# Optimization experiments

Hardware: AMD Instinct MI355X
Metric: run time of the kernel (lower is better)

Reference implementation:

```python
import jax, jax.numpy as jnp
import numpy as np

T, B, S, L = 256, 128, 256, 2
H, E, V = 512, 512, 32000


def setup_inputs() -> dict:
    key = jax.random.key(0)
    ks = jax.random.split(key, 17)
    n = lambda k, shape, s=0.05: jax.random.normal(k, shape, dtype=jnp.float32) * s
    tokens = jax.random.randint(ks[0], (T, B), 0, V)
    emb = n(ks[1], (V, E)).at[0].set(0.0)  # padding_idx=0 row zeroed
    return {
        "tokens": tokens,
        "h0": n(ks[2], (L, B, H)),
        "c0": n(ks[3], (L, B, H)),
        "context": n(ks[4], (S, B, H)),
        "init_output": n(ks[5], (B, H)),
        "emb": emb,
        "W_ih0": n(ks[6], (4 * H, E + H)),
        "b_ih0": n(ks[7], (4 * H,)),
        "W_hh0": n(ks[8], (4 * H, H)),
        "b_hh0": n(ks[9], (4 * H,)),
        "W_ih1": n(ks[10], (4 * H, H)),
        "b_ih1": n(ks[11], (4 * H,)),
        "W_hh1": n(ks[12], (4 * H, H)),
        "b_hh1": n(ks[13], (4 * H,)),
        "W_in": n(ks[14], (H, H)),
        "W_out": n(ks[15], (H, 2 * H)),
    }


def _lstm_cell(x, h, c, Wi, bi, Wh, bh):
    # torch LSTMCell: gates ordered i, f, g, o
    g = x @ Wi.T + bi + h @ Wh.T + bh
    i, f, gg, o = jnp.split(g, 4, axis=-1)
    c2 = jax.nn.sigmoid(f) * c + jax.nn.sigmoid(i) * jnp.tanh(gg)
    h2 = jax.nn.sigmoid(o) * jnp.tanh(c2)
    return h2, c2


def reference(tokens, h0, c0, context, init_output, emb,
              W_ih0, b_ih0, W_hh0, b_hh0, W_ih1, b_ih1, W_hh1, b_hh1,
              W_in, W_out):
    emb_seq = emb[tokens]                      # [T, B, E]
    ctx = jnp.transpose(context, (1, 0, 2))    # [B, S, H] (context.transpose(0,1))

    def step(carry, e_t):
        h, c, out = carry                      # h,c: [L,B,H]; out: [B,H]
        x = jnp.concatenate([e_t, out], axis=1)  # input feed
        h0_, c0_ = _lstm_cell(x, h[0], c[0], W_ih0, b_ih0, W_hh0, b_hh0)
        h1_, c1_ = _lstm_cell(h0_, h[1], c[1], W_ih1, b_ih1, W_hh1, b_hh1)
        rnn_out = h1_                          # dropout is identity at p=0 / eval
        # GlobalAttention (Luong general): score = ctx @ (W_in h)
        q = rnn_out @ W_in.T                   # [B, H]
        scores = jnp.einsum('bsh,bh->bs', ctx, q)
        a = jax.nn.softmax(scores, axis=-1)    # [B, S]
        wc = jnp.einsum('bs,bsh->bh', a, ctx)  # weighted context
        attn_out = jnp.tanh(jnp.concatenate([wc, rnn_out], axis=1) @ W_out.T)
        new_h = jnp.stack([h0_, h1_])
        new_c = jnp.stack([c0_, c1_])
        return (new_h, new_c, attn_out), (attn_out, a)

    (hF, cF, _), (outputs, attns) = jax.lax.scan(step, (h0, c0, init_output), emb_seq)
    return outputs, hF, cF, attns[-1]
```

## Files before the change

### kernel.cpp

```cpp
#include <hip/hip_runtime.h>
#include <hip/hip_bf16.h>
#include <math.h>

#define TT 256
#define BB 128
#define SS 256
#define HH 512
#define EE 512
#define NBLK 128
#define NTHR 512
#define BH (BB * HH)

typedef __attribute__((ext_vector_type(4))) float f32x4;
typedef __attribute__((ext_vector_type(2))) float f32x2;
typedef __attribute__((ext_vector_type(8))) short s16x8;
typedef unsigned long long u64;

__device__ __forceinline__ float b2f(short v) {
    union { unsigned u; float f; } c;
    c.u = ((unsigned)(unsigned short)v) << 16;
    return c.f;
}
__device__ __forceinline__ short f2b(float f) {
    union { float f; unsigned u; } c; c.f = f;
    unsigned u = c.u;
    unsigned r = (u + 0x7fffu + ((u >> 16) & 1u)) >> 16;
    return (short)r;
}
__device__ __forceinline__ float sigm(float x) { return 1.f / (1.f + __expf(-x)); }

__device__ __forceinline__ unsigned short f2fp8x2(float x, float y) {
    return (unsigned short)(__builtin_amdgcn_cvt_pk_fp8_f32(x, y, 0, false) & 0xffff);
}
__device__ __forceinline__ void f8x8(u64 q, float* o) {
    unsigned w0 = (unsigned)q, w1 = (unsigned)(q >> 32);
    f32x2 a = __builtin_amdgcn_cvt_pk_f32_fp8(w0, false);
    f32x2 b = __builtin_amdgcn_cvt_pk_f32_fp8(w0, true);
    f32x2 c = __builtin_amdgcn_cvt_pk_f32_fp8(w1, false);
    f32x2 d = __builtin_amdgcn_cvt_pk_f32_fp8(w1, true);
    o[0] = a[0]; o[1] = a[1]; o[2] = b[0]; o[3] = b[1];
    o[4] = c[0]; o[5] = c[1]; o[6] = d[0]; o[7] = d[1];
}

__device__ __forceinline__ u64 aldq(const void* p) {
    return __hip_atomic_load((const u64*)p, __ATOMIC_RELAXED, __HIP_MEMORY_SCOPE_AGENT);
}
__device__ __forceinline__ void ast2(short* p, short v) {
    __hip_atomic_store(p, v, __ATOMIC_RELAXED, __HIP_MEMORY_SCOPE_AGENT);
}
__device__ __forceinline__ s16x8 ald16(const void* p) {
    s16x8 r;
    asm volatile("global_load_dwordx4 %0, %1, off sc0 sc1" : "=v"(r) : "v"(p) : "memory");
    return r;
}


__global__ void k_pack2(const float* __restrict__ Wa, int ka, const float* __restrict__ Wb, int kb,
                        short* __restrict__ dst, int n) {
    const int K = ka + kb;
    for (int i = blockIdx.x * blockDim.x + threadIdx.x; i < n; i += gridDim.x * blockDim.x) {
        int g = i / K, k = i - g * K;
        float v = (k < ka) ? Wa[(size_t)g * ka + k] : Wb[(size_t)g * kb + (k - ka)];
        dst[i] = f2b(v);
    }
}

__global__ void k_bias(const float* __restrict__ a, const float* __restrict__ b, float* __restrict__ o,
                       const float* __restrict__ a2, const float* __restrict__ b2, float* __restrict__ o2) {
    int i = blockIdx.x * blockDim.x + threadIdx.x;
    if (i < 2048) { o[i] = a[i] + b[i]; o2[i] = a2[i] + b2[i]; }
}

__global__ void k_emb(const int* __restrict__ tok, const float* __restrict__ emb, short* __restrict__ Ebf) {
    const int n = TT * BB * EE;
    for (int i = blockIdx.x * blockDim.x + threadIdx.x; i < n; i += gridDim.x * blockDim.x) {
        int tb = i >> 9, k = i & 511;
        int t = tok[tb];
        Ebf[i] = f2b(emb[(size_t)t * EE + k]);
    }
}

__global__ void k_ctx8(const float* __restrict__ ctx, unsigned char* __restrict__ c8) {
    const int n2 = BB * SS * (HH / 2);
    for (int i = blockIdx.x * blockDim.x + threadIdx.x; i < n2; i += gridDim.x * blockDim.x) {
        int h2 = i & 255, rest = i >> 8;
        int s = rest & 255, b = rest >> 8;
        int h = h2 * 2;
        const float* src = ctx + ((size_t)s * BB + b) * HH + h;
        *reinterpret_cast<unsigned short*>(c8 + ((size_t)b * SS + s) * HH + h) = f2fp8x2(src[0], src[1]);
    }
}

__global__ __launch_bounds__(512) void k_ctxw8(const float* __restrict__ ctx, const short* __restrict__ Winb,
                                               unsigned char* __restrict__ ctxW8) {
    const int tid = threadIdx.x, w = tid >> 6, l = tid & 63;
    const int m0 = blockIdx.y * 128, n0 = blockIdx.x * 64;
    const int kc8 = (l >> 4) * 8;
    const int m = m0 + w * 16 + (l & 15);
    const int b = m >> 8, s = m & 255;
    const float* arow = ctx + ((size_t)s * BB + b) * HH + kc8;
    f32x4 acc[4];
    const f32x4 zero = {0.f, 0.f, 0.f, 0.f};
#pragma unroll
    for (int j = 0; j < 4; ++j) acc[j] = zero;
#pragma unroll
    for (int kc = 0; kc < 16; ++kc) {
        const int k0 = kc * 32;
        float4 x0 = *reinterpret_cast<const float4*>(arow + k0);
        float4 x1 = *reinterpret_cast<const float4*>(arow + k0 + 4);
        s16x8 afr;
        afr[0] = f2b(x0.x); afr[1] = f2b(x0.y); afr[2] = f2b(x0.z); afr[3] = f2b(x0.w);
        afr[4] = f2b(x1.x); afr[5] = f2b(x1.y); afr[6] = f2b(x1.z); afr[7] = f2b(x1.w);
#pragma unroll
        for (int j = 0; j < 4; ++j) {
            s16x8 bfr = *reinterpret_cast<const s16x8*>(Winb + (size_t)(n0 + j * 16 + (l & 15)) * HH + k0 + kc8);
            acc[j] = __builtin_amdgcn_mfma_f32_16x16x32_bf16(afr, bfr, acc[j], 0, 0, 0);
        }
    }
#pragma unroll
    for (int j = 0; j < 4; ++j)
#pragma unroll
        for (int r = 0; r < 4; ++r)
            ctxW8[(size_t)(m0 + w * 16 + (l >> 4) * 4 + r) * HH + (n0 + j * 16 + (l & 15))] =
                (unsigned char)(__builtin_amdgcn_cvt_pk_fp8_f32(acc[j][r], 0.f, 0, false) & 0xff);
}

__global__ void k_state(const float* __restrict__ h0in, const float* __restrict__ iout,
                        short* __restrict__ h0x, short* __restrict__ h1x, short* __restrict__ outx) {
    int i = blockIdx.x * blockDim.x + threadIdx.x;
    if (i < BH) {
        h0x[i] = f2b(h0in[i]);
        h1x[i] = f2b(h0in[BH + i]);
        outx[i] = f2b(iout[i]);
    }
}


struct P {
    const short* Ebf;
    const float* c0in;
    const unsigned char* ctxb8;
    const unsigned char* ctxW8;
    const short* W0cat;
    const short* W1cat;
    const short* Woutb;
    const float* bias0;
    const float* bias1;
    short* h0x;
    short* h1x;
    short* outx;
    short* wcx;
    float* dout;
    unsigned* flags;
};

#define MFMA16(a, b, c) __builtin_amdgcn_mfma_f32_16x16x32_bf16((a), (b), (c), 0, 0, 0)

__device__ __forceinline__ s16x8 ldsfrag(const short* base, int stride, int row, int col8) {
    return *reinterpret_cast<const s16x8*>(base + row * stride + ((col8 ^ (row & 7)) << 3));
}

__device__ __forceinline__ void issue8(const short* __restrict__ src, int tid, int khalf, s16x8* q) {
#pragma unroll
    for (int c = 0; c < 8; ++c) {
        const int chunk = c * 512 + tid;
        const int row = chunk >> 5, col8 = chunk & 31;
        q[c] = ald16(src + row * HH + khalf * 256 + col8 * 8);
    }
}
__device__ __forceinline__ void write8(short* __restrict__ stg, int tid, const s16x8* q) {
    asm volatile("s_waitcnt vmcnt(0)" ::: "memory");
#pragma unroll
    for (int c = 0; c < 8; ++c) {
        const int chunk = c * 512 + tid;
        const int row = chunk >> 5, col8 = chunk & 31;
        *reinterpret_cast<s16x8*>(stg + row * 256 + ((col8 ^ (row & 7)) << 3)) = q[c];
    }
}

__device__ __forceinline__ f32x4 seg8(const short* stgp, const short* Ws, int wstride, int wbase,
                                      int mrow, int wrow, int kq, f32x4 acc) {
#pragma unroll
    for (int seg = 0; seg < 8; ++seg)
        acc = MFMA16(ldsfrag(stgp, 256, mrow, seg * 4 + kq),
                     ldsfrag(Ws, wstride, wrow, wbase + seg * 4 + kq), acc);
    return acc;
}

__device__ __forceinline__ f32x4 seg8m(const short* stgp, const short* Wd, int wbase,
                                       int mrow, int nn, int kq, bool valid, f32x4 acc) {
    const s16x8 zz = {0, 0, 0, 0, 0, 0, 0, 0};
#pragma unroll
    for (int seg = 0; seg < 8; ++seg) {
        s16x8 b = ldsfrag(Wd, 1024, nn & 3, wbase + seg * 4 + kq);
        if (!valid) b = zz;
        acc = MFMA16(ldsfrag(stgp, 256, mrow, seg * 4 + kq), b, acc);
    }
    return acc;
}

__device__ __forceinline__ void gbar(unsigned* flags, unsigned target) {
    asm volatile("s_waitcnt vmcnt(0)" ::: "memory");
    __syncthreads();
    if (threadIdx.x == 0)
        __hip_atomic_store(&flags[blockIdx.x], target, __ATOMIC_RELAXED, __HIP_MEMORY_SCOPE_AGENT);
    if (threadIdx.x < NBLK) {
        while (__hip_atomic_load(&flags[threadIdx.x], __ATOMIC_RELAXED, __HIP_MEMORY_SCOPE_AGENT) < target)
            __builtin_amdgcn_s_sleep(1);
    }
    __syncthreads();
}

__global__ void __launch_bounds__(NTHR, 1) coop_k(P p) {
    extern __shared__ __align__(16) char smem[];
    short* W0s = (short*)smem;
    short* W1s = W0s + 16 * 1536;
    short* Wds = W1s + 16 * 1024;
    short* stg = Wds + 4 * 1024;
    float* smallf = (float*)(stg + 128 * 256);
    float* bias0s = smallf;
    float* bias1s = smallf + 16;
    float* red = smallf + 32;
    float* scv = smallf + 48;
    float* aU = smallf + 304;

    const int tid = threadIdx.x;
    const int blk = blockIdx.x;
    const int l = tid & 63;
    const int w = tid >> 6;
    const int lrow = l & 15;
    const int mrow = w * 16 + lrow;
    const int kq = l >> 4;
    const size_t OFF_HF = (size_t)TT * BH;
    const size_t OFF_CF = OFF_HF + 2 * (size_t)BH;
    const size_t OFF_AT = OFF_CF + 2 * (size_t)BH;
    const f32x4 fz = {0.f, 0.f, 0.f, 0.f};

    for (int idx = tid; idx < 16 * 192; idx += NTHR) {
        int row = idx / 192, col8 = idx % 192;
        int g = (row & 3) * 512 + blk * 4 + (row >> 2);
        *reinterpret_cast<s16x8*>(W0s + row * 1536 + ((col8 ^ (row & 7)) << 3)) =
            *reinterpret_cast<const s16x8*>(p.W0cat + (size_t)g * 1536 + col8 * 8);
    }
    for (int idx = tid; idx < 16 * 128; idx += NTHR) {
        int row = idx / 128, col8 = idx % 128;
        int g = (row & 3) * 512 + blk * 4 + (row >> 2);
        *reinterpret_cast<s16x8*>(W1s + row * 1024 + ((col8 ^ (row & 7)) << 3)) =
            *reinterpret_cast<const s16x8*>(p.W1cat + (size_t)g * 1024 + col8 * 8);
    }
    {
        int row = tid >> 7, col8 = tid & 127;
        *reinterpret_cast<s16x8*>(Wds + row * 1024 + ((col8 ^ row) << 3)) =
            *reinterpret_cast<const s16x8*>(p.Woutb + (size_t)(blk * 4 + row) * 1024 + col8 * 8);
    }
    if (tid < 16) {
        int g = (tid & 3) * 512 + blk * 4 + (tid >> 2);
        bias0s[tid] = p.bias0[g];
        bias1s[tid] = p.bias1[g];
    }
    __syncthreads();

    const int bA = tid >> 2;
    const int jA = blk * 4 + (tid & 3);
    float c0reg = p.c0in[bA * HH + jA];
    float c1reg = p.c0in[BH + bA * HH + jA];
    unsigned ep = 0;
    s16x8 qa[8], qb[8];

    for (int t = 0; t < TT; ++t) {
        const size_t pB = (size_t)(t & 1) * BH;
        const size_t pN = (size_t)((t & 1) ^ 1) * BH;

        {
            issue8(p.outx + pB, tid, 0, qa);
            f32x4 aE = fz, aO = fz, aH = fz;
            {
                const short* erow = p.Ebf + ((size_t)t * BB + mrow) * EE + kq * 8;
#pragma unroll
                for (int seg = 0; seg < 16; ++seg) {
                    s16x8 afr = *reinterpret_cast<const s16x8*>(erow + seg * 32);
                    aE = MFMA16(afr, ldsfrag(W0s, 1536, lrow, seg * 4 + kq), aE);
                }
            }
            write8(stg, tid, qa);
            issue8(p.outx + pB, tid, 1, qb);
            __syncthreads();
            aO = seg8(stg, W0s, 1536, 64, mrow, lrow, kq, aO);
            __syncthreads();
            write8(stg, tid, qb);
            issue8(p.h0x + pB, tid, 0, qa);
            __syncthreads();
            aO = seg8(stg, W0s, 1536, 96, mrow, lrow, kq, aO);
            __syncthreads();
            write8(stg, tid, qa);
            issue8(p.h0x + pB, tid, 1, qb);
            __syncthreads();
            aH = seg8(stg, W0s, 1536, 128, mrow, lrow, kq, aH);
            __syncthreads();
            write8(stg, tid, qb);
            __syncthreads();
            aH = seg8(stg, W0s, 1536, 160, mrow, lrow, kq, aH);

            f32x4 acc = aE + aO + aH;
            __syncthreads();
            float* scr = (float*)stg + w * 272;
#pragma unroll
            for (int r = 0; r < 4; ++r) scr[lrow * 17 + kq * 4 + r] = acc[r];
            __syncthreads();
            const int bloc = l >> 2;
            const int n0 = (l & 3) * 4;
            float gi = scr[(n0 + 0) * 17 + bloc] + bias0s[n0 + 0];
            float gf = scr[(n0 + 1) * 17 + bloc] + bias0s[n0 + 1];
            float gg = scr[(n0 + 2) * 17 + bloc] + bias0s[n0 + 2];
            float go = scr[(n0 + 3) * 17 + bloc] + bias0s[n0 + 3];
            float cn = sigm(gf) * c0reg + sigm(gi) * tanhf(gg);
            float hn = sigm(go) * tanhf(cn);
            c0reg = cn;
            ast2(&p.h0x[pN + bA * HH + jA], f2b(hn));
            if (t == TT - 1) {
                p.dout[OFF_HF + bA * HH + jA] = hn;
                p.dout[OFF_CF + bA * HH + jA] = cn;
            }
        }
        gbar(p.flags, ++ep);

        {
            issue8(p.h0x + pN, tid, 0, qa);
            f32x4 b0 = fz, b1 = fz;
            write8(stg, tid, qa);
            issue8(p.h0x + pN, tid, 1, qb);
            __syncthreads();
            b0 = seg8(stg, W1s, 1024, 0, mrow, lrow, kq, b0);
            __syncthreads();
            write8(stg, tid, qb);
            issue8(p.h1x + pB, tid, 0, qa);
            __syncthreads();
            b0 = seg8(stg, W1s, 1024, 32, mrow, lrow, kq, b0);
            __syncthreads();
            write8(stg, tid, qa);
            issue8(p.h1x + pB, tid, 1, qb);
            __syncthreads();
            b1 = seg8(stg, W1s, 1024, 64, mrow, lrow, kq, b1);
            __syncthreads();
            write8(stg, tid, qb);
            __syncthreads();
            b1 = seg8(stg, W1s, 1024, 96, mrow, lrow, kq, b1);

            f32x4 acc = b0 + b1;
            __syncthreads();
            float* scr = (float*)stg + w * 272;
#pragma unroll
            for (int r = 0; r < 4; ++r) scr[lrow * 17 + kq * 4 + r] = acc[r];
            __syncthreads();
            const int bloc = l >> 2;
            const int n0 = (l & 3) * 4;
            float gi = scr[(n0 + 0) * 17 + bloc] + bias1s[n0 + 0];
            float gf = scr[(n0 + 1) * 17 + bloc] + bias1s[n0 + 1];
            float gg = scr[(n0 + 2) * 17 + bloc] + bias1s[n0 + 2];
            float go = scr[(n0 + 3) * 17 + bloc] + bias1s[n0 + 3];
            float cn = sigm(gf) * c1reg + sigm(gi) * tanhf(gg);
            float hn = sigm(go) * tanhf(cn);
            c1reg = cn;
            ast2(&p.h1x[pN + bA * HH + jA], f2b(hn));
            if (t == TT - 1) {
                p.dout[OFF_HF + BH + bA * HH + jA] = hn;
                p.dout[OFF_CF + BH + bA * HH + jA] = cn;
            }
        }
        gbar(p.flags, ++ep);

        {
            float* pF = (float*)stg;
            float* h1f = pF + 4096;
            if (tid < 128) {
                union { u64 v; short s[4]; } c;
                c.v = aldq(p.h1x + pN + blk * HH + tid * 4);
#pragma unroll
                for (int j = 0; j < 4; ++j) h1f[tid * 4 + j] = b2f(c.s[j]);
            }
            __syncthreads();
            float hreg[8];
#pragma unroll
            for (int j = 0; j < 8; ++j) hreg[j] = h1f[l * 8 + j];
            const unsigned char* cwb = p.ctxW8 + (size_t)blk * SS * HH;
#pragma unroll 4
            for (int it = 0; it < 32; ++it) {
                const int s = it * 8 + w;
                u64 q = *reinterpret_cast<const u64*>(cwb + (size_t)s * HH + l * 8);
                float o[8];
                f8x8(q, o);
                float pd = 0.f;
#pragma unroll
                for (int j = 0; j < 8; ++j) pd += o[j] * hreg[j];
#pragma unroll
                for (int off = 32; off; off >>= 1) pd += __shfl_xor(pd, off);
                if (l == 0) scv[s] = pd;
            }
            __syncthreads();
            float sc = -1e30f, e = 0.f;
            if (tid < 256) sc = scv[tid];
            float mx = sc;
#pragma unroll
            for (int off = 32; off; off >>= 1) mx = fmaxf(mx, __shfl_xor(mx, off));
            if (l == 0 && tid < 256) red[w] = mx;
            __syncthreads();
            const float M = fmaxf(fmaxf(red[0], red[1]), fmaxf(red[2], red[3]));
            if (tid < 256) { e = __expf(sc - M); aU[tid] = e; }
            float se = e;
#pragma unroll
            for (int off = 32; off; off >>= 1) se += __shfl_xor(se, off);
            if (l == 0 && tid < 256) red[8 + w] = se;
            __syncthreads();
            const float inv = 1.f / (red[8] + red[9] + red[10] + red[11]);
            if (t == TT - 1 && tid < 256) p.dout[OFF_AT + blk * SS + tid] = aU[tid] * inv;
            const unsigned char* cbb = p.ctxb8 + (size_t)blk * SS * HH;
            float wa[8];
#pragma unroll
            for (int j = 0; j < 8; ++j) wa[j] = 0.f;
#pragma unroll 4
            for (int it = 0; it < 32; ++it) {
                const int s = it * 8 + w;
                const float av = aU[s];
                u64 q = *reinterpret_cast<const u64*>(cbb + (size_t)s * HH + l * 8);
                float o[8];
                f8x8(q, o);
#pragma unroll
                for (int j = 0; j < 8; ++j) wa[j] += av * o[j];
            }
            {
                float4* dst = reinterpret_cast<float4*>(pF + w * 512 + l * 8);
                float4 v0 = {wa[0], wa[1], wa[2], wa[3]};
                float4 v1 = {wa[4], wa[5], wa[6], wa[7]};
                dst[0] = v0;
                dst[1] = v1;
            }
            __syncthreads();
            float s8 = 0.f;
#pragma unroll
            for (int ww = 0; ww < 8; ++ww) s8 += pF[ww * 512 + tid];
            ast2(&p.wcx[blk * HH + tid], f2b(s8 * inv));
        }
        gbar(p.flags, ++ep);

        {
            issue8(p.wcx, tid, 0, qa);
            f32x4 acc = fz;
            const int nn = l & 15;
            const bool dv = nn < 4;
            write8(stg, tid, qa);
            issue8(p.wcx, tid, 1, qb);
            __syncthreads();
            acc = seg8m(stg, Wds, 0, mrow, nn, kq, dv, acc);
            __syncthreads();
            write8(stg, tid, qb);
            issue8(p.h1x + pN, tid, 0, qa);
            __syncthreads();
            acc = seg8m(stg, Wds, 32, mrow, nn, kq, dv, acc);
            __syncthreads();
            write8(stg, tid, qa);
            issue8(p.h1x + pN, tid, 1, qb);
            __syncthreads();
            acc = seg8m(stg, Wds, 64, mrow, nn, kq, dv, acc);
            __syncthreads();
            write8(stg, tid, qb);
            __syncthreads();
            acc = seg8m(stg, Wds, 96, mrow, nn, kq, dv, acc);
            if (dv) {
                const int col = blk * 4 + nn;
#pragma unroll
                for (int r = 0; r < 4; ++r) {
                    const int row = w * 16 + (l >> 4) * 4 + r;
                    float tv = tanhf(acc[r]);
                    __builtin_nontemporal_store(tv, &p.dout[(size_t)t * BH + row * HH + col]);
                    ast2(&p.outx[pN + row * HH + col], f2b(tv));
                }
            }
        }
        gbar(p.flags, ++ep);
    }
}


extern "C" void kernel_launch(void* const* d_in, const int* in_sizes, int n_in,
                              void* d_out, int out_size, void* d_ws, size_t ws_size,
                              hipStream_t stream) {
    const int* tokens = (const int*)d_in[0];
    const float* h0in = (const float*)d_in[1];
    const float* c0in = (const float*)d_in[2];
    const float* ctx = (const float*)d_in[3];
    const float* iout = (const float*)d_in[4];
    const float* emb = (const float*)d_in[5];
    const float* Wih0 = (const float*)d_in[6];
    const float* bih0 = (const float*)d_in[7];
    const float* Whh0 = (const float*)d_in[8];
    const float* bhh0 = (const float*)d_in[9];
    const float* Wih1 = (const float*)d_in[10];
    const float* bih1 = (const float*)d_in[11];
    const float* Whh1 = (const float*)d_in[12];
    const float* bhh1 = (const float*)d_in[13];
    const float* Win = (const float*)d_in[14];
    const float* Wout = (const float*)d_in[15];
    float* dout = (float*)d_out;

    char* pw = (char*)d_ws;
    auto take = [&](size_t bytes) { char* r = pw; pw += (bytes + 255) & ~(size_t)255; return r; };
    short* W0cat = (short*)take((size_t)2048 * 1536 * 2);
    short* W1cat = (short*)take((size_t)2048 * 1024 * 2);
    short* Winb  = (short*)take((size_t)512 * 512 * 2);
    short* Woutb = (short*)take((size_t)512 * 1024 * 2);
    float* bias0 = (float*)take(2048 * 4);
    float* bias1 = (float*)take(2048 * 4);
    short* Ebf   = (short*)take((size_t)TT * BB * EE * 2);
    unsigned char* ctxb8 = (unsigned char*)take((size_t)BB * SS * HH);
    unsigned char* ctxW8 = (unsigned char*)take((size_t)BB * SS * HH);
    short* h0x   = (short*)take((size_t)2 * BH * 2);
    short* h1x   = (short*)take((size_t)2 * BH * 2);
    short* outx  = (short*)take((size_t)2 * BH * 2);
    short* wcx   = (short*)take((size_t)BH * 2);
    unsigned* flags = (unsigned*)take(NBLK * 4);

    k_pack2<<<2048, 256, 0, stream>>>(Wih0, 1024, Whh0, 512, W0cat, 2048 * 1536);
    k_pack2<<<2048, 256, 0, stream>>>(Wih1, 512, Whh1, 512, W1cat, 2048 * 1024);
    k_pack2<<<1024, 256, 0, stream>>>(Win, 512, Win, 0, Winb, 512 * 512);
    k_pack2<<<1024, 256, 0, stream>>>(Wout, 1024, Wout, 0, Woutb, 512 * 1024);
    k_bias<<<8, 256, 0, stream>>>(bih0, bhh0, bias0, bih1, bhh1, bias1);
    k_emb<<<4096, 256, 0, stream>>>(tokens, emb, Ebf);
    k_ctx8<<<4096, 256, 0, stream>>>(ctx, ctxb8);
    k_state<<<256, 256, 0, stream>>>(h0in, iout, h0x, h1x, outx);
    k_ctxw8<<<dim3(8, 256), 512, 0, stream>>>(ctx, Winb, ctxW8);
    (void)hipMemsetAsync(flags, 0, NBLK * 4, stream);

    const unsigned smem_bytes = (16 * 1536 + 16 * 1024 + 4 * 1024 + 128 * 256) * 2 + (16 + 16 + 16 + 256 + 256) * 4;
    (void)hipFuncSetAttribute((const void*)coop_k, hipFuncAttributeMaxDynamicSharedMemorySize, (int)smem_bytes);

    P prm;
    prm.Ebf = Ebf; prm.c0in = c0in;
    prm.ctxb8 = ctxb8; prm.ctxW8 = ctxW8;
    prm.W0cat = W0cat; prm.W1cat = W1cat; prm.Woutb = Woutb;
    prm.bias0 = bias0; prm.bias1 = bias1;
    prm.h0x = h0x; prm.h1x = h1x; prm.outx = outx; prm.wcx = wcx;
    prm.dout = dout; prm.flags = flags;
    void* args[] = {&prm};
    (void)hipLaunchCooperativeKernel((void*)coop_k, dim3(NBLK), dim3(NTHR), args, smem_bytes, stream);
}
```

Measured before the change: 15.08 ms.

## Precompute ctx·W_out context projection to drop one grid barrier per step

The context half of the output projection is folded into a precomputed fp8 tensor, ctx @ W_out[:, :H].T, built by the generalized k_cvt8 kernel. Each block now forms its batch row's attention output directly as the attention-weighted sum of this projected context plus an h1·W_out_r dot product read from a packed bf16 buffer. This removes the separate output-projection phase and its grid-wide barrier each timestep. It also replaces many __syncthreads with lighter LDS-only barriers and prefetches more global loads ahead of time, at the cost of more precomputed memory and extra fp8 quantization error.

```diff
diff --git a/kernel.cpp b/kernel.cpp
--- a/kernel.cpp
+++ b/kernel.cpp
@@ -54,6 +54,11 @@
     return r;
 }
 
+__device__ __forceinline__ void lbar() {
+    asm volatile("s_waitcnt lgkmcnt(0)" ::: "memory");
+    __builtin_amdgcn_s_barrier();
+}
+
 
 __global__ void k_pack2(const float* __restrict__ Wa, int ka, const float* __restrict__ Wb, int kb,
                         short* __restrict__ dst, int n) {
@@ -80,19 +85,18 @@
     }
 }
 
-__global__ void k_ctx8(const float* __restrict__ ctx, unsigned char* __restrict__ c8) {
-    const int n2 = BB * SS * (HH / 2);
-    for (int i = blockIdx.x * blockDim.x + threadIdx.x; i < n2; i += gridDim.x * blockDim.x) {
-        int h2 = i & 255, rest = i >> 8;
-        int s = rest & 255, b = rest >> 8;
-        int h = h2 * 2;
-        const float* src = ctx + ((size_t)s * BB + b) * HH + h;
-        *reinterpret_cast<unsigned short*>(c8 + ((size_t)b * SS + s) * HH + h) = f2fp8x2(src[0], src[1]);
-    }
-}
-
-__global__ __launch_bounds__(512) void k_ctxw8(const float* __restrict__ ctx, const short* __restrict__ Winb,
-                                               unsigned char* __restrict__ ctxW8) {
+__global__ void k_packwr(const float* __restrict__ Wout, unsigned* __restrict__ WRP) {
+    int i = blockIdx.x * blockDim.x + threadIdx.x;
+    if (i < 256 * 512) {
+        int m = i >> 9, j = i & 511;
+        unsigned lo = (unsigned)(unsigned short)f2b(Wout[(size_t)j * 1024 + 512 + 2 * m]);
+        unsigned hi = (unsigned)(unsigned short)f2b(Wout[(size_t)j * 1024 + 512 + 2 * m + 1]);
+        WRP[i] = lo | (hi << 16);
+    }
+}
+
+__global__ __launch_bounds__(512) void k_cvt8(const float* __restrict__ ctx, const short* __restrict__ Wb,
+                                              int wstride, unsigned char* __restrict__ out8) {
     const int tid = threadIdx.x, w = tid >> 6, l = tid & 63;
     const int m0 = blockIdx.y * 128, n0 = blockIdx.x * 64;
     const int kc8 = (l >> 4) * 8;
@@ -113,7 +117,7 @@
         afr[4] = f2b(x1.x); afr[5] = f2b(x1.y); afr[6] = f2b(x1.z); afr[7] = f2b(x1.w);
 #pragma unroll
         for (int j = 0; j < 4; ++j) {
-            s16x8 bfr = *reinterpret_cast<const s16x8*>(Winb + (size_t)(n0 + j * 16 + (l & 15)) * HH + k0 + kc8);
+            s16x8 bfr = *reinterpret_cast<const s16x8*>(Wb + (size_t)(n0 + j * 16 + (l & 15)) * wstride + k0 + kc8);
             acc[j] = __builtin_amdgcn_mfma_f32_16x16x32_bf16(afr, bfr, acc[j], 0, 0, 0);
         }
     }
@@ -121,7 +125,7 @@
     for (int j = 0; j < 4; ++j)
 #pragma unroll
         for (int r = 0; r < 4; ++r)
-            ctxW8[(size_t)(m0 + w * 16 + (l >> 4) * 4 + r) * HH + (n0 + j * 16 + (l & 15))] =
+            out8[(size_t)(m0 + w * 16 + (l >> 4) * 4 + r) * HH + (n0 + j * 16 + (l & 15))] =
                 (unsigned char)(__builtin_amdgcn_cvt_pk_fp8_f32(acc[j][r], 0.f, 0, false) & 0xff);
 }
 
@@ -139,17 +143,16 @@
 struct P {
     const short* Ebf;
     const float* c0in;
-    const unsigned char* ctxb8;
     const unsigned char* ctxW8;
+    const unsigned char* ctxO8;
+    const unsigned* WRP;
     const short* W0cat;
     const short* W1cat;
-    const short* Woutb;
     const float* bias0;
     const float* bias1;
     short* h0x;
     short* h1x;
     short* outx;
-    short* wcx;
     float* dout;
     unsigned* flags;
 };
@@ -168,8 +171,9 @@
         q[c] = ald16(src + row * HH + khalf * 256 + col8 * 8);
     }
 }
-__device__ __forceinline__ void write8(short* __restrict__ stg, int tid, const s16x8* q) {
-    asm volatile("s_waitcnt vmcnt(0)" ::: "memory");
+template <int N>
+__device__ __forceinline__ void write8n(short* __restrict__ stg, int tid, const s16x8* q) {
+    asm volatile("s_waitcnt vmcnt(%0)" ::"i"(N) : "memory");
 #pragma unroll
     for (int c = 0; c < 8; ++c) {
         const int chunk = c * 512 + tid;
@@ -184,18 +188,6 @@
     for (int seg = 0; seg < 8; ++seg)
         acc = MFMA16(ldsfrag(stgp, 256, mrow, seg * 4 + kq),
                      ldsfrag(Ws, wstride, wrow, wbase + seg * 4 + kq), acc);
-    return acc;
-}
-
-__device__ __forceinline__ f32x4 seg8m(const short* stgp, const short* Wd, int wbase,
-                                       int mrow, int nn, int kq, bool valid, f32x4 acc) {
-    const s16x8 zz = {0, 0, 0, 0, 0, 0, 0, 0};
-#pragma unroll
-    for (int seg = 0; seg < 8; ++seg) {
-        s16x8 b = ldsfrag(Wd, 1024, nn & 3, wbase + seg * 4 + kq);
-        if (!valid) b = zz;
-        acc = MFMA16(ldsfrag(stgp, 256, mrow, seg * 4 + kq), b, acc);
-    }
     return acc;
 }
 
@@ -215,14 +207,14 @@
     extern __shared__ __align__(16) char smem[];
     short* W0s = (short*)smem;
     short* W1s = W0s + 16 * 1536;
-    short* Wds = W1s + 16 * 1024;
-    short* stg = Wds + 4 * 1024;
+    short* stg = W1s + 16 * 1024;
     float* smallf = (float*)(stg + 128 * 256);
     float* bias0s = smallf;
     float* bias1s = smallf + 16;
     float* red = smallf + 32;
     float* scv = smallf + 48;
     float* aU = smallf + 304;
+    float* h1f = smallf + 560;
 
     const int tid = threadIdx.x;
     const int blk = blockIdx.x;
@@ -248,11 +240,6 @@
         *reinterpret_cast<s16x8*>(W1s + row * 1024 + ((col8 ^ (row & 7)) << 3)) =
             *reinterpret_cast<const s16x8*>(p.W1cat + (size_t)g * 1024 + col8 * 8);
     }
-    {
-        int row = tid >> 7, col8 = tid & 127;
-        *reinterpret_cast<s16x8*>(Wds + row * 1024 + ((col8 ^ row) << 3)) =
-            *reinterpret_cast<const s16x8*>(p.Woutb + (size_t)(blk * 4 + row) * 1024 + col8 * 8);
-    }
     if (tid < 16) {
         int g = (tid & 3) * 512 + blk * 4 + (tid >> 2);
         bias0s[tid] = p.bias0[g];
@@ -265,7 +252,7 @@
     float c0reg = p.c0in[bA * HH + jA];
     float c1reg = p.c0in[BH + bA * HH + jA];
     unsigned ep = 0;
-    s16x8 qa[8], qb[8];
+    s16x8 qa[8], qb[8], qc[8], qd[8];
 
     for (int t = 0; t < TT; ++t) {
         const size_t pB = (size_t)(t & 1) * BH;
@@ -273,6 +260,7 @@
 
         {
             issue8(p.outx + pB, tid, 0, qa);
+            issue8(p.outx + pB, tid, 1, qb);
             f32x4 aE = fz, aO = fz, aH = fz;
             {
                 const short* erow = p.Ebf + ((size_t)t * BB + mrow) * EE + kq * 8;
@@ -282,31 +270,29 @@
                     aE = MFMA16(afr, ldsfrag(W0s, 1536, lrow, seg * 4 + kq), aE);
                 }
             }
-            write8(stg, tid, qa);
-            issue8(p.outx + pB, tid, 1, qb);
-            __syncthreads();
+            write8n<8>(stg, tid, qa);
+            issue8(p.h0x + pB, tid, 0, qc);
+            lbar();
             aO = seg8(stg, W0s, 1536, 64, mrow, lrow, kq, aO);
-            __syncthreads();
-            write8(stg, tid, qb);
-            issue8(p.h0x + pB, tid, 0, qa);
-            __syncthreads();
+            lbar();
+            write8n<8>(stg, tid, qb);
+            issue8(p.h0x + pB, tid, 1, qd);
+            lbar();
             aO = seg8(stg, W0s, 1536, 96, mrow, lrow, kq, aO);
-            __syncthreads();
-            write8(stg, tid, qa);
-            issue8(p.h0x + pB, tid, 1, qb);
-            __syncthreads();
+            lbar();
+            write8n<8>(stg, tid, qc);
+            lbar();
             aH = seg8(stg, W0s, 1536, 128, mrow, lrow, kq, aH);
-            __syncthreads();
-            write8(stg, tid, qb);
-            __syncthreads();
+            lbar();
+            write8n<0>(stg, tid, qd);
+            lbar();
             aH = seg8(stg, W0s, 1536, 160, mrow, lrow, kq, aH);
 
             f32x4 acc = aE + aO + aH;
-            __syncthreads();
+            lbar();
             float* scr = (float*)stg + w * 272;
 #pragma unroll
             for (int r = 0; r < 4; ++r) scr[lrow * 17 + kq * 4 + r] = acc[r];
-            __syncthreads();
             const int bloc = l >> 2;
             const int n0 = (l & 3) * 4;
             float gi = scr[(n0 + 0) * 17 + bloc] + bias0s[n0 + 0];
@@ -326,32 +312,31 @@
 
         {
             issue8(p.h0x + pN, tid, 0, qa);
+            issue8(p.h0x + pN, tid, 1, qb);
             f32x4 b0 = fz, b1 = fz;
-            write8(stg, tid, qa);
-            issue8(p.h0x + pN, tid, 1, qb);
-            __syncthreads();
+            write8n<8>(stg, tid, qa);
+            issue8(p.h1x + pB, tid, 0, qc);
+            lbar();
             b0 = seg8(stg, W1s, 1024, 0, mrow, lrow, kq, b0);
-            __syncthreads();
-            write8(stg, tid, qb);
-            issue8(p.h1x + pB, tid, 0, qa);
-            __syncthreads();
+            lbar();
+            write8n<8>(stg, tid, qb);
+            issue8(p.h1x + pB, tid, 1, qd);
+            lbar();
             b0 = seg8(stg, W1s, 1024, 32, mrow, lrow, kq, b0);
-            __syncthreads();
-            write8(stg, tid, qa);
-            issue8(p.h1x + pB, tid, 1, qb);
-            __syncthreads();
+            lbar();
+            write8n<8>(stg, tid, qc);
+            lbar();
             b1 = seg8(stg, W1s, 1024, 64, mrow, lrow, kq, b1);
-            __syncthreads();
-            write8(stg, tid, qb);
-            __syncthreads();
+            lbar();
+            write8n<0>(stg, tid, qd);
+            lbar();
             b1 = seg8(stg, W1s, 1024, 96, mrow, lrow, kq, b1);
 
             f32x4 acc = b0 + b1;
-            __syncthreads();
+            lbar();
             float* scr = (float*)stg + w * 272;
 #pragma unroll
             for (int r = 0; r < 4; ++r) scr[lrow * 17 + kq * 4 + r] = acc[r];
-            __syncthreads();
             const int bloc = l >> 2;
             const int n0 = (l & 3) * 4;
             float gi = scr[(n0 + 0) * 17 + bloc] + bias1s[n0 + 0];
@@ -371,14 +356,13 @@
 
         {
             float* pF = (float*)stg;
-            float* h1f = pF + 4096;
             if (tid < 128) {
                 union { u64 v; short s[4]; } c;
                 c.v = aldq(p.h1x + pN + blk * HH + tid * 4);
 #pragma unroll
                 for (int j = 0; j < 4; ++j) h1f[tid * 4 + j] = b2f(c.s[j]);
             }
-            __syncthreads();
+            lbar();
             float hreg[8];
 #pragma unroll
             for (int j = 0; j < 8; ++j) hreg[j] = h1f[l * 8 + j];
@@ -396,24 +380,24 @@
                 for (int off = 32; off; off >>= 1) pd += __shfl_xor(pd, off);
                 if (l == 0) scv[s] = pd;
             }
-            __syncthreads();
+            lbar();
             float sc = -1e30f, e = 0.f;
             if (tid < 256) sc = scv[tid];
             float mx = sc;
 #pragma unroll
             for (int off = 32; off; off >>= 1) mx = fmaxf(mx, __shfl_xor(mx, off));
             if (l == 0 && tid < 256) red[w] = mx;
-            __syncthreads();
+            lbar();
             const float M = fmaxf(fmaxf(red[0], red[1]), fmaxf(red[2], red[3]));
             if (tid < 256) { e = __expf(sc - M); aU[tid] = e; }
             float se = e;
 #pragma unroll
             for (int off = 32; off; off >>= 1) se += __shfl_xor(se, off);
             if (l == 0 && tid < 256) red[8 + w] = se;
-            __syncthreads();
+            lbar();
             const float inv = 1.f / (red[8] + red[9] + red[10] + red[11]);
             if (t == TT - 1 && tid < 256) p.dout[OFF_AT + blk * SS + tid] = aU[tid] * inv;
-            const unsigned char* cbb = p.ctxb8 + (size_t)blk * SS * HH;
+            const unsigned char* cob = p.ctxO8 + (size_t)blk * SS * HH;
             float wa[8];
 #pragma unroll
             for (int j = 0; j < 8; ++j) wa[j] = 0.f;
@@ -421,7 +405,7 @@
             for (int it = 0; it < 32; ++it) {
                 const int s = it * 8 + w;
                 const float av = aU[s];
-                u64 q = *reinterpret_cast<const u64*>(cbb + (size_t)s * HH + l * 8);
+                u64 q = *reinterpret_cast<const u64*>(cob + (size_t)s * HH + l * 8);
                 float o[8];
                 f8x8(q, o);
 #pragma unroll
@@ -434,46 +418,22 @@
                 dst[0] = v0;
                 dst[1] = v1;
             }
-            __syncthreads();
-            float s8 = 0.f;
-#pragma unroll
-            for (int ww = 0; ww < 8; ++ww) s8 += pF[ww * 512 + tid];
-            ast2(&p.wcx[blk * HH + tid], f2b(s8 * inv));
-        }
-        gbar(p.flags, ++ep);
-
-        {
-            issue8(p.wcx, tid, 0, qa);
-            f32x4 acc = fz;
-            const int nn = l & 15;
-            const bool dv = nn < 4;
-            write8(stg, tid, qa);
-            issue8(p.wcx, tid, 1, qb);
-            __syncthreads();
-            acc = seg8m(stg, Wds, 0, mrow, nn, kq, dv, acc);
-            __syncthreads();
-            write8(stg, tid, qb);
-            issue8(p.h1x + pN, tid, 0, qa);
-            __syncthreads();
-            acc = seg8m(stg, Wds, 32, mrow, nn, kq, dv, acc);
-            __syncthreads();
-            write8(stg, tid, qa);
-            issue8(p.h1x + pN, tid, 1, qb);
-            __syncthreads();
-            acc = seg8m(stg, Wds, 64, mrow, nn, kq, dv, acc);
-            __syncthreads();
-            write8(stg, tid, qb);
-            __syncthreads();
-            acc = seg8m(stg, Wds, 96, mrow, nn, kq, dv, acc);
-            if (dv) {
-                const int col = blk * 4 + nn;
-#pragma unroll
-                for (int r = 0; r < 4; ++r) {
-                    const int row = w * 16 + (l >> 4) * 4 + r;
-                    float tv = tanhf(acc[r]);
-                    __builtin_nontemporal_store(tv, &p.dout[(size_t)t * BH + row * HH + col]);
-                    ast2(&p.outx[pN + row * HH + col], f2b(tv));
+            lbar();
+            {
+                float opv = 0.f;
+#pragma unroll
+                for (int ww = 0; ww < 8; ++ww) opv += pF[ww * 512 + tid];
+                opv *= inv;
+                const unsigned* wp = p.WRP + tid;
+                float g = 0.f;
+#pragma unroll 8
+                for (int m = 0; m < 256; ++m) {
+                    unsigned wv = wp[(size_t)m * 512];
+                    g += b2f((short)(wv & 0xffff)) * h1f[2 * m] + b2f((short)(wv >> 16)) * h1f[2 * m + 1];
                 }
+                float tv = tanhf(opv + g);
+                __builtin_nontemporal_store(tv, &p.dout[(size_t)t * BH + blk * HH + tid]);
+                ast2(&p.outx[pN + blk * HH + tid], f2b(tv));
             }
         }
         gbar(p.flags, ++ep);
@@ -508,37 +468,38 @@
     short* W1cat = (short*)take((size_t)2048 * 1024 * 2);
     short* Winb  = (short*)take((size_t)512 * 512 * 2);
     short* Woutb = (short*)take((size_t)512 * 1024 * 2);
+    unsigned* WRP = (unsigned*)take((size_t)256 * 512 * 4);
     float* bias0 = (float*)take(2048 * 4);
     float* bias1 = (float*)take(2048 * 4);
     short* Ebf   = (short*)take((size_t)TT * BB * EE * 2);
-    unsigned char* ctxb8 = (unsigned char*)take((size_t)BB * SS * HH);
     unsigned char* ctxW8 = (unsigned char*)take((size_t)BB * SS * HH);
+    unsigned char* ctxO8 = (unsigned char*)take((size_t)BB * SS * HH);
     short* h0x   = (short*)take((size_t)2 * BH * 2);
     short* h1x   = (short*)take((size_t)2 * BH * 2);
     short* outx  = (short*)take((size_t)2 * BH * 2);
-    short* wcx   = (short*)take((size_t)BH * 2);
     unsigned* flags = (unsigned*)take(NBLK * 4);
 
     k_pack2<<<2048, 256, 0, stream>>>(Wih0, 1024, Whh0, 512, W0cat, 2048 * 1536);
     k_pack2<<<2048, 256, 0, stream>>>(Wih1, 512, Whh1, 512, W1cat, 2048 * 1024);
     k_pack2<<<1024, 256, 0, stream>>>(Win, 512, Win, 0, Winb, 512 * 512);
     k_pack2<<<1024, 256, 0, stream>>>(Wout, 1024, Wout, 0, Woutb, 512 * 1024);
+    k_packwr<<<512, 256, 0, stream>>>(Wout, WRP);
     k_bias<<<8, 256, 0, stream>>>(bih0, bhh0, bias0, bih1, bhh1, bias1);
     k_emb<<<4096, 256, 0, stream>>>(tokens, emb, Ebf);
-    k_ctx8<<<4096, 256, 0, stream>>>(ctx, ctxb8);
     k_state<<<256, 256, 0, stream>>>(h0in, iout, h0x, h1x, outx);
-    k_ctxw8<<<dim3(8, 256), 512, 0, stream>>>(ctx, Winb, ctxW8);
+    k_cvt8<<<dim3(8, 256), 512, 0, stream>>>(ctx, Winb, 512, ctxW8);
+    k_cvt8<<<dim3(8, 256), 512, 0, stream>>>(ctx, Woutb, 1024, ctxO8);
     (void)hipMemsetAsync(flags, 0, NBLK * 4, stream);
 
-    const unsigned smem_bytes = (16 * 1536 + 16 * 1024 + 4 * 1024 + 128 * 256) * 2 + (16 + 16 + 16 + 256 + 256) * 4;
+    const unsigned smem_bytes = (16 * 1536 + 16 * 1024 + 128 * 256) * 2 + (16 + 16 + 16 + 256 + 256 + 512) * 4;
     (void)hipFuncSetAttribute((const void*)coop_k, hipFuncAttributeMaxDynamicSharedMemorySize, (int)smem_bytes);
 
     P prm;
     prm.Ebf = Ebf; prm.c0in = c0in;
-    prm.ctxb8 = ctxb8; prm.ctxW8 = ctxW8;
-    prm.W0cat = W0cat; prm.W1cat = W1cat; prm.Woutb = Woutb;
+    prm.ctxW8 = ctxW8; prm.ctxO8 = ctxO8; prm.WRP = WRP;
+    prm.W0cat = W0cat; prm.W1cat = W1cat;
     prm.bias0 = bias0; prm.bias1 = bias1;
-    prm.h0x = h0x; prm.h1x = h1x; prm.outx = outx; prm.wcx = wcx;
+    prm.h0x = h0x; prm.h1x = h1x; prm.outx = outx;
     prm.dout = dout; prm.flags = flags;
     void* args[] = {&prm};
     (void)hipLaunchCooperativeKernel((void*)coop_k, dim3(NBLK), dim3(NTHR), args, smem_bytes, stream);
```

New measurement: 14.80 ms. No clear change (-1.9%).
